# Optimization experiments

Hardware: AMD Instinct MI355X
Metric: run time of the kernel (lower is better)

The kernel has to match this reference:

```python
import jax, jax.numpy as jnp
import numpy as np
from jax import lax

B, S, H, E, F, K = 4, 2048, 1024, 8, 4096, 2

def setup_inputs() -> dict:
    key = jax.random.key(0)
    k1, k2, k3, k4 = jax.random.split(key, 4)
    return {
        "hidden_states": jax.random.normal(k1, (B, S, H), dtype=jnp.float32),
        "router_logits": jax.random.normal(k2, (B, S, E), dtype=jnp.float32),
        "w1": jax.random.normal(k3, (E, H, F), dtype=jnp.float32) * 0.02,
        "w2": jax.random.normal(k4, (E, F, H), dtype=jnp.float32) * 0.02,
        "layer_idx": 0,
    }


def reference(hidden_states, router_logits, w1, w2, layer_idx):
    b, s, h = hidden_states.shape
    e = router_logits.shape[-1]
    T = b * s
    x = hidden_states.reshape(T, h)              # [T, H] flattened tokens
    logits = router_logits.reshape(T, e)          # [T, E]

    # top-k routing, softmax over the selected k scores (as in torch.topk + softmax)
    topk_scores, topk_idx = lax.top_k(logits, K)  # [T, K]
    probs = jax.nn.softmax(topk_scores, axis=-1)  # [T, K]

    # scatter combine weights into a dense [T, E] map (dispatch weights)
    cw = jnp.zeros((T, e), dtype=probs.dtype).at[jnp.arange(T)[:, None], topk_idx].add(probs)

    # grouped expert compute: scan over experts, masked weighted accumulation
    def step(acc, ew):
        w1e, w2e, ce = ew                          # [H,F], [F,H], [T]
        he = jax.nn.gelu(x @ w1e) @ w2e            # [T, H] expert FFN
        return acc + ce[:, None] * he, None

    out, _ = lax.scan(step, jnp.zeros_like(x), (w1, w2, cw.T))
    return out.reshape(b, s, h)
```

## Files before the change

kernel.cpp:

```cpp
#include <hip/hip_runtime.h>

#define T_TOKENS 8192
#define H_DIM 1024
#define E_EXP 8
#define F_DIM 4096
#define CAP 8192
#define MT_TILES 32

typedef __attribute__((ext_vector_type(8))) short short8;
typedef __attribute__((ext_vector_type(8))) unsigned short ushort8;
typedef __attribute__((ext_vector_type(4))) float f32x4;

__device__ __forceinline__ unsigned short f2bf(float f) {
    unsigned int u = __float_as_uint(f);
    u += 0x7fffu + ((u >> 16) & 1u);
    return (unsigned short)(u >> 16);
}

__device__ __forceinline__ float gelu_tanh(float x) {
    float z = 0.7978845608028654f * (x + 0.044715f * x * x * x);
    float t = 1.0f - 2.0f / (__expf(2.0f * z) + 1.0f);
    return 0.5f * x * (1.0f + t);
}

__device__ __forceinline__ void gld16(const void* g, void* l) {
    __builtin_amdgcn_global_load_lds(
        (const __attribute__((address_space(1))) unsigned int*)g,
        (__attribute__((address_space(3))) unsigned int*)l,
        16, 0, 0);
}

__global__ void router_kernel(const float* __restrict__ logits,
                              int* __restrict__ cnt,
                              int* __restrict__ tok,
                              float* __restrict__ wt) {
    int t = blockIdx.x * 256 + threadIdx.x;
    if (t >= T_TOKENS) return;
    float l[E_EXP];
#pragma unroll
    for (int i = 0; i < E_EXP; i++) l[i] = logits[t * E_EXP + i];
    int i0 = 0; float s0 = l[0];
#pragma unroll
    for (int i = 1; i < E_EXP; i++) if (l[i] > s0) { s0 = l[i]; i0 = i; }
    int i1 = (i0 == 0) ? 1 : 0; float s1 = l[i1];
#pragma unroll
    for (int i = 0; i < E_EXP; i++) if (i != i0 && l[i] > s1) { s1 = l[i]; i1 = i; }
    float p0 = 1.0f / (1.0f + __expf(s1 - s0));
    float p1 = 1.0f - p0;
    int sl0 = atomicAdd(&cnt[i0], 1);
    tok[i0 * CAP + sl0] = t; wt[i0 * CAP + sl0] = p0;
    int sl1 = atomicAdd(&cnt[i1], 1);
    tok[i1 * CAP + sl1] = t; wt[i1 * CAP + sl1] = p1;
}

__global__ void base_kernel(const int* __restrict__ cnt, int* __restrict__ base) {
    if (threadIdx.x == 0) {
        int b = 0;
        for (int e = 0; e < E_EXP; e++) { base[e] = b; b += cnt[e]; }
    }
}

__global__ void cvtx_kernel(const float* __restrict__ x, unsigned short* __restrict__ xg) {
    int i = blockIdx.x * 256 + threadIdx.x;
    float4 v = ((const float4*)x)[i];
    ushort4 o;
    o.x = f2bf(v.x); o.y = f2bf(v.y); o.z = f2bf(v.z); o.w = f2bf(v.w);
    ((ushort4*)xg)[i] = o;
}

__global__ void tcvt_kernel(const float* __restrict__ in, unsigned short* __restrict__ out,
                            int M, int N) {
    __shared__ float t[64][65];
    size_t eoff = (size_t)blockIdx.z * M * N;
    in += eoff; out += eoff;
    int r0 = blockIdx.x * 64, c0 = blockIdx.y * 64;
    int tid = threadIdx.x;
    int srow = tid >> 4;
    int scol = (tid & 15) * 4;
#pragma unroll
    for (int p = 0; p < 4; p++) {
        int row = p * 16 + srow;
        float4 v = *(const float4*)&in[(size_t)(r0 + row) * N + c0 + scol];
        t[row][scol + 0] = v.x; t[row][scol + 1] = v.y;
        t[row][scol + 2] = v.z; t[row][scol + 3] = v.w;
    }
    __syncthreads();
    int orow = tid >> 3;
    int ocb = (tid & 7) * 8;
#pragma unroll
    for (int p = 0; p < 2; p++) {
        int r = p * 32 + orow;
        ushort8 o;
#pragma unroll
        for (int i = 0; i < 8; i++) o[i] = f2bf(t[ocb + i][r]);
        *(ushort8*)&out[(size_t)(c0 + r) * M + r0 + ocb] = o;
    }
}

template <int GATHER, int EPI, int NT8>
__global__ __launch_bounds__(256, 2)
void gemm_kernel(const unsigned short* __restrict__ Asrc,
                 const unsigned short* __restrict__ Bt,
                 int K, int N,
                 const int* __restrict__ cnt, const int* __restrict__ base,
                 const int* __restrict__ tok, const float* __restrict__ wt,
                 unsigned short* __restrict__ Gout, float* __restrict__ out) {
    int bid = blockIdx.x;
    int xcd = bid & 7;
    int q = bid >> 3;
    int nl = q % NT8;
    int q2 = q / NT8;
    int m_tile = q2 & (MT_TILES - 1);
    const int e = q2 >> 5;
    const int n_tile = xcd * NT8 + nl;

    const int cnt_e = cnt[e];
    const int m0 = m_tile * 128;
    if (m0 >= cnt_e) return;
    const int base_e = base[e];
    const int n0 = n_tile * 128;
    const int tid = threadIdx.x;
    const int lane = tid & 63;
    const int wave = tid >> 6;
    const int quad = lane >> 4, l16 = lane & 15;
    const int wm = (wave & 1) * 64, wn = (wave >> 1) * 64;

    __shared__ unsigned short As[2][128][32];
    __shared__ unsigned short Bs[2][128][32];

    const int srow = wave * 16 + (lane >> 2);
    const int selem = (lane & 3) * 8;
    const unsigned short* aptr[2];
    const unsigned short* bptr[2];
#pragma unroll
    for (int p = 0; p < 2; p++) {
        int gr = m0 + p * 64 + srow;
        if (gr > cnt_e - 1) gr = cnt_e - 1;
        const unsigned short* arow;
        if (GATHER) arow = Asrc + (size_t)tok[e * CAP + gr] * K;
        else        arow = Asrc + (size_t)(base_e + gr) * K;
        aptr[p] = arow + selem;
        bptr[p] = Bt + (size_t)e * (size_t)N * K + (size_t)(n0 + p * 64 + srow) * K + selem;
    }
    unsigned short* alds0 = &As[0][wave * 16][0];
    unsigned short* alds1 = &As[0][64 + wave * 16][0];
    unsigned short* blds0 = &Bs[0][wave * 16][0];
    unsigned short* blds1 = &Bs[0][64 + wave * 16][0];
    const int HALF = 128 * 32;

    f32x4 acc[4][4];
#pragma unroll
    for (int i = 0; i < 4; i++)
#pragma unroll
        for (int j = 0; j < 4; j++) acc[i][j] = (f32x4){0.f, 0.f, 0.f, 0.f};

    for (int k0 = 0; k0 < K; k0 += 64) {
#pragma unroll
        for (int sub = 0; sub < 2; sub++) {
            gld16(aptr[0] + k0 + sub * 32, alds0 + sub * HALF);
            gld16(aptr[1] + k0 + sub * 32, alds1 + sub * HALF);
            gld16(bptr[0] + k0 + sub * 32, blds0 + sub * HALF);
            gld16(bptr[1] + k0 + sub * 32, blds1 + sub * HALF);
        }
        __syncthreads();
#pragma unroll
        for (int sub = 0; sub < 2; sub++) {
            short8 af[4], bf[4];
#pragma unroll
            for (int i = 0; i < 4; i++)
                af[i] = *(const short8*)&As[sub][wm + i * 16 + l16][quad * 8];
#pragma unroll
            for (int j = 0; j < 4; j++)
                bf[j] = *(const short8*)&Bs[sub][wn + j * 16 + l16][quad * 8];
#pragma unroll
            for (int i = 0; i < 4; i++)
#pragma unroll
                for (int j = 0; j < 4; j++)
                    acc[i][j] = __builtin_amdgcn_mfma_f32_16x16x32_bf16(af[i], bf[j], acc[i][j], 0, 0, 0);
        }
        __syncthreads();
    }

    if (EPI == 0) {
#pragma unroll
        for (int i = 0; i < 4; i++) {
            int lm = wm + i * 16 + quad * 4;
#pragma unroll
            for (int r = 0; r < 4; r++) {
                int gr = m0 + lm + r;
                if (gr < cnt_e) {
                    size_t rowoff = (size_t)(base_e + gr) * N;
#pragma unroll
                    for (int j = 0; j < 4; j++) {
                        int ncol = n0 + wn + j * 16 + l16;
                        Gout[rowoff + ncol] = f2bf(gelu_tanh(acc[i][j][r]));
                    }
                }
            }
        }
    } else {
#pragma unroll
        for (int i = 0; i < 4; i++) {
            int lm = wm + i * 16 + quad * 4;
#pragma unroll
            for (int r = 0; r < 4; r++) {
                int gr = m0 + lm + r;
                if (gr < cnt_e) {
                    int tk = tok[e * CAP + gr];
                    float w = wt[e * CAP + gr];
                    float* orow = out + (size_t)tk * N;
#pragma unroll
                    for (int j = 0; j < 4; j++) {
                        int ncol = n0 + wn + j * 16 + l16;
                        atomicAdd(&orow[ncol], w * acc[i][j][r]);
                    }
                }
            }
        }
    }
}

extern "C" void kernel_launch(void* const* d_in, const int* in_sizes, int n_in,
                              void* d_out, int out_size, void* d_ws, size_t ws_size,
                              hipStream_t stream) {
    const float* x      = (const float*)d_in[0];
    const float* logits = (const float*)d_in[1];
    const float* w1     = (const float*)d_in[2];
    const float* w2     = (const float*)d_in[3];
    float* out = (float*)d_out;
    char* ws = (char*)d_ws;

    const size_t OFF_CNT  = 0;
    const size_t OFF_BASE = 64;
    const size_t OFF_TOK  = 1024;
    const size_t OFF_WT   = OFF_TOK + (size_t)E_EXP * CAP * 4;
    const size_t OFF_XG   = 1u << 20;
    const size_t OFF_W1T  = OFF_XG + (size_t)T_TOKENS * H_DIM * 2;
    const size_t OFF_W2T  = OFF_W1T + (size_t)E_EXP * H_DIM * F_DIM * 2;
    const size_t OFF_G    = OFF_W2T + (size_t)E_EXP * H_DIM * F_DIM * 2;

    int* cnt  = (int*)(ws + OFF_CNT);
    int* base = (int*)(ws + OFF_BASE);
    int* tok  = (int*)(ws + OFF_TOK);
    float* wt = (float*)(ws + OFF_WT);
    unsigned short* xg  = (unsigned short*)(ws + OFF_XG);
    unsigned short* w1t = (unsigned short*)(ws + OFF_W1T);
    unsigned short* w2t = (unsigned short*)(ws + OFF_W2T);
    unsigned short* G   = (unsigned short*)(ws + OFF_G);

    hipMemsetAsync(d_out, 0, (size_t)out_size * sizeof(float), stream);
    hipMemsetAsync(cnt, 0, 64, stream);

    router_kernel<<<T_TOKENS / 256, 256, 0, stream>>>(logits, cnt, tok, wt);
    base_kernel<<<1, 64, 0, stream>>>(cnt, base);
    cvtx_kernel<<<(T_TOKENS * H_DIM / 4) / 256, 256, 0, stream>>>(x, xg);
    tcvt_kernel<<<dim3(H_DIM / 64, F_DIM / 64, E_EXP), 256, 0, stream>>>(w1, w1t, H_DIM, F_DIM);
    tcvt_kernel<<<dim3(F_DIM / 64, H_DIM / 64, E_EXP), 256, 0, stream>>>(w2, w2t, F_DIM, H_DIM);
    gemm_kernel<1, 0, 4><<<8 * 4 * MT_TILES * E_EXP, 256, 0, stream>>>(
        xg, w1t, H_DIM, F_DIM, cnt, base, tok, wt, G, nullptr);
    gemm_kernel<0, 1, 1><<<8 * 1 * MT_TILES * E_EXP, 256, 0, stream>>>(
        G, w2t, F_DIM, H_DIM, cnt, base, tok, wt, nullptr, out);
    (void)in_sizes; (void)n_in; (void)ws_size;
}
```

Before: 819.2 us.

## Aggregate router atomics per block and remap GEMM2 tiles across XCDs

The router now counts expert assignments in shared memory and issues one global atomic per expert per block, instead of one per token-slot. The GEMM gains an MC parameter that spreads M tiles across XCD groups, and the second GEMM uses MC=2 with two N tiles per XCD. The intent is better L2 reuse and load balance across XCDs for the down projection. Launch bounds rise from 2 to 4 blocks per CU, which tightens the register budget and may cause spills.

Result: faster. 748.4 us (-8.6%).

```diff
diff --git a/kernel.cpp b/kernel.cpp
--- a/kernel.cpp
+++ b/kernel.cpp
@@ -34,8 +34,12 @@
                               int* __restrict__ cnt,
                               int* __restrict__ tok,
                               float* __restrict__ wt) {
-    int t = blockIdx.x * 256 + threadIdx.x;
-    if (t >= T_TOKENS) return;
+    __shared__ int hcnt[E_EXP];
+    __shared__ int hbase[E_EXP];
+    int tid = threadIdx.x;
+    if (tid < E_EXP) hcnt[tid] = 0;
+    __syncthreads();
+    int t = blockIdx.x * 256 + tid;
     float l[E_EXP];
 #pragma unroll
     for (int i = 0; i < E_EXP; i++) l[i] = logits[t * E_EXP + i];
@@ -47,9 +51,14 @@
     for (int i = 0; i < E_EXP; i++) if (i != i0 && l[i] > s1) { s1 = l[i]; i1 = i; }
     float p0 = 1.0f / (1.0f + __expf(s1 - s0));
     float p1 = 1.0f - p0;
-    int sl0 = atomicAdd(&cnt[i0], 1);
+    int lo0 = atomicAdd(&hcnt[i0], 1);
+    int lo1 = atomicAdd(&hcnt[i1], 1);
+    __syncthreads();
+    if (tid < E_EXP) hbase[tid] = atomicAdd(&cnt[tid], hcnt[tid]);
+    __syncthreads();
+    int sl0 = hbase[i0] + lo0;
     tok[i0 * CAP + sl0] = t; wt[i0 * CAP + sl0] = p0;
-    int sl1 = atomicAdd(&cnt[i1], 1);
+    int sl1 = hbase[i1] + lo1;
     tok[i1 * CAP + sl1] = t; wt[i1 * CAP + sl1] = p1;
 }
 
@@ -97,8 +106,8 @@
     }
 }
 
-template <int GATHER, int EPI, int NT8>
-__global__ __launch_bounds__(256, 2)
+template <int GATHER, int EPI, int NT8, int MC>
+__global__ __launch_bounds__(256, 4)
 void gemm_kernel(const unsigned short* __restrict__ Asrc,
                  const unsigned short* __restrict__ Bt,
                  int K, int N,
@@ -110,9 +119,12 @@
     int q = bid >> 3;
     int nl = q % NT8;
     int q2 = q / NT8;
-    int m_tile = q2 & (MT_TILES - 1);
-    const int e = q2 >> 5;
-    const int n_tile = xcd * NT8 + nl;
+    const int MTG = MT_TILES / MC;
+    int mt = q2 % MTG;
+    const int e = q2 / MTG;
+    const int g = xcd & (MC - 1);
+    const int n_tile = (xcd / MC) * NT8 + nl;
+    const int m_tile = mt * MC + g;
 
     const int cnt_e = cnt[e];
     const int m0 = m_tile * 128;
@@ -256,9 +268,9 @@
     cvtx_kernel<<<(T_TOKENS * H_DIM / 4) / 256, 256, 0, stream>>>(x, xg);
     tcvt_kernel<<<dim3(H_DIM / 64, F_DIM / 64, E_EXP), 256, 0, stream>>>(w1, w1t, H_DIM, F_DIM);
     tcvt_kernel<<<dim3(F_DIM / 64, H_DIM / 64, E_EXP), 256, 0, stream>>>(w2, w2t, F_DIM, H_DIM);
-    gemm_kernel<1, 0, 4><<<8 * 4 * MT_TILES * E_EXP, 256, 0, stream>>>(
+    gemm_kernel<1, 0, 4, 1><<<8 * 4 * MT_TILES * E_EXP, 256, 0, stream>>>(
         xg, w1t, H_DIM, F_DIM, cnt, base, tok, wt, G, nullptr);
-    gemm_kernel<0, 1, 1><<<8 * 1 * MT_TILES * E_EXP, 256, 0, stream>>>(
+    gemm_kernel<0, 1, 2, 2><<<8 * 2 * (MT_TILES / 2) * E_EXP, 256, 0, stream>>>(
         G, w2t, F_DIM, H_DIM, cnt, base, tok, wt, nullptr, out);
     (void)in_sizes; (void)n_in; (void)ws_size;
 }
```
